# Kernel optimization log

Measured on AMD Instinct MI355X. Metric: run time of the kernel, lower is better.

The kernel has to match this reference:

```python
import jax, jax.numpy as jnp
import numpy as np

NUM_HEADS = 8
WIN = 7  # local_window_size
HALF = WIN // 2


def setup_inputs() -> dict:
    key = jax.random.key(0)
    k1, k2, k3 = jax.random.split(key, 3)
    B, N, C = 1, 4096, 384  # N = T*H*W with T=4, H=W=32
    x = jax.random.normal(k1, (B, N, C), dtype=jnp.float32)
    w_qkv = jax.random.normal(k2, (C, 3 * C), dtype=jnp.float32) * 0.02
    w_proj = jax.random.normal(k3, (C, C), dtype=jnp.float32) * 0.02
    b_proj = jnp.zeros((C,), dtype=jnp.float32)
    return {"x": x, "w_qkv": w_qkv, "w_proj": w_proj, "b_proj": b_proj, "H": 32, "W": 32}


def _gather_windows(t):
    H, W = t.shape[3], t.shape[4]
    tp = jnp.pad(t, ((0, 0), (0, 0), (0, 0), (HALF, HALF), (HALF, HALF), (0, 0)))
    wins = [tp[:, :, :, dy:dy + H, dx:dx + W, :] for dy in range(WIN) for dx in range(WIN)]
    return jnp.stack(wins, axis=5)


def reference(x, w_qkv, w_proj, b_proj, H, W):
    B, N, C = x.shape
    nh, hd = NUM_HEADS, C // NUM_HEADS
    T = N // (H * W)
    scale = hd ** (-0.5)

    qkv = (x @ w_qkv).reshape(B, N, 3, nh, hd)
    # (B, nh, T, H, W, hd)
    q = qkv[:, :, 0].transpose(0, 2, 1, 3).reshape(B, nh, T, H, W, hd)
    k = qkv[:, :, 1].transpose(0, 2, 1, 3).reshape(B, nh, T, H, W, hd)
    v = qkv[:, :, 2].transpose(0, 2, 1, 3).reshape(B, nh, T, H, W, hd)

    kwin = _gather_windows(k)  # (B, nh, T, H, W, 49, hd); zeros at borders (NOT masked)
    vwin = _gather_windows(v)

    scores = jnp.einsum('bnthwd,bnthwkd->bnthwk', q, kwin) * scale
    attn = jax.nn.softmax(scores, axis=-1)  # zero-padded keys give score 0 -> weight exp(0)
    out = jnp.einsum('bnthwk,bnthwkd->bnthwd', attn, vwin)

    out = out.transpose(0, 2, 3, 4, 1, 5).reshape(B, N, C)
    return out @ w_proj + b_proj
```

## Files before the change

kernel.cpp:

```cpp
#include <hip/hip_runtime.h>
#include <hip/hip_bf16.h>
#include <math.h>

#define NH 8
#define HD 48
#define C_DIM 384
#define C3 1152
#define SCALE_F 0.14433756729740643f

typedef unsigned short ushort_t;
typedef __attribute__((ext_vector_type(8))) short short8;
typedef __attribute__((ext_vector_type(4))) float f32x4;

static __device__ __forceinline__ ushort_t bf16u(float f) {
    __hip_bfloat16 b = __float2bfloat16(f);
    return *(ushort_t*)&b;
}

__global__ __launch_bounds__(256) void split_bf16_kernel(const float* __restrict__ in,
                                                         ushort_t* __restrict__ hi,
                                                         ushort_t* __restrict__ lo,
                                                         int n4)
{
    const int i = blockIdx.x * 256 + threadIdx.x;
    if (i >= n4) return;
    const float4 v = ((const float4*)in)[i];
    const float f[4] = {v.x, v.y, v.z, v.w};
    ushort_t hb[4], lb[4];
    #pragma unroll
    for (int j = 0; j < 4; ++j) {
        __hip_bfloat16 h = __float2bfloat16(f[j]);
        __hip_bfloat16 l = __float2bfloat16(f[j] - __bfloat162float(h));
        hb[j] = *(ushort_t*)&h;
        lb[j] = *(ushort_t*)&l;
    }
    *(ushort4*)(hi + i * 4) = make_ushort4(hb[0], hb[1], hb[2], hb[3]);
    *(ushort4*)(lo + i * 4) = make_ushort4(lb[0], lb[1], lb[2], lb[3]);
}

__global__ __launch_bounds__(256) void split_wT_kernel(const float* __restrict__ w,
                                                       ushort_t* __restrict__ hiT,
                                                       ushort_t* __restrict__ loT,
                                                       int K, int N)
{
    const int idx = blockIdx.x * 256 + threadIdx.x;
    if (idx >= K * N) return;
    const int k = idx / N;
    const int n = idx - k * N;
    const float v = w[idx];
    __hip_bfloat16 h = __float2bfloat16(v);
    __hip_bfloat16 l = __float2bfloat16(v - __bfloat162float(h));
    hiT[n * K + k] = *(ushort_t*)&h;
    loT[n * K + k] = *(ushort_t*)&l;
}

__global__ __launch_bounds__(256) void gemm_mfma3(const ushort_t* __restrict__ Ah,
                                                  const ushort_t* __restrict__ Al,
                                                  const ushort_t* __restrict__ BhT,
                                                  const ushort_t* __restrict__ BlT,
                                                  const float* __restrict__ bias,
                                                  float* __restrict__ C,
                                                  int N, int K)
{
    __shared__ ushort_t sAh[128 * 40];
    __shared__ ushort_t sAl[128 * 40];
    __shared__ ushort_t sBh[64 * 40];
    __shared__ ushort_t sBl[64 * 40];

    const int tid = threadIdx.x;
    const int bm = blockIdx.x * 128;
    const int bn = blockIdx.y * 64;

    const int rowA = tid >> 2;
    const int slotA = (tid & 3) * 8;
    const int rowB = tid >> 2;
    const int slotB = (tid & 3) * 8;

    const ushort_t* gAh0 = Ah + (size_t)(bm + rowA) * K + slotA;
    const ushort_t* gAh1 = Ah + (size_t)(bm + rowA + 64) * K + slotA;
    const ushort_t* gAl0 = Al + (size_t)(bm + rowA) * K + slotA;
    const ushort_t* gAl1 = Al + (size_t)(bm + rowA + 64) * K + slotA;
    const ushort_t* gBh  = BhT + (size_t)(bn + rowB) * K + slotB;
    const ushort_t* gBl  = BlT + (size_t)(bn + rowB) * K + slotB;

    const int lane = tid & 63;
    const int wid = tid >> 6;
    const int wm = wid >> 1;
    const int wn = wid & 1;
    const int fr = lane & 15;
    const int kb = lane >> 4;
    const int aoff = (wm * 64 + fr) * 40 + kb * 8;
    const int boff = (wn * 32 + fr) * 40 + kb * 8;

    f32x4 acc[4][2] = {};

    for (int k0 = 0; k0 < K; k0 += 32) {
        const short8 va0 = *(const short8*)(gAh0 + k0);
        const short8 va1 = *(const short8*)(gAh1 + k0);
        const short8 vl0 = *(const short8*)(gAl0 + k0);
        const short8 vl1 = *(const short8*)(gAl1 + k0);
        const short8 vb0 = *(const short8*)(gBh + k0);
        const short8 vb1 = *(const short8*)(gBl + k0);
        *(short8*)&sAh[rowA * 40 + slotA]        = va0;
        *(short8*)&sAh[(rowA + 64) * 40 + slotA] = va1;
        *(short8*)&sAl[rowA * 40 + slotA]        = vl0;
        *(short8*)&sAl[(rowA + 64) * 40 + slotA] = vl1;
        *(short8*)&sBh[rowB * 40 + slotB]        = vb0;
        *(short8*)&sBl[rowB * 40 + slotB]        = vb1;
        __syncthreads();

        short8 ah[4], al[4], bh[2], bl[2];
        #pragma unroll
        for (int m = 0; m < 4; ++m) {
            ah[m] = *(const short8*)&sAh[aoff + m * 16 * 40];
            al[m] = *(const short8*)&sAl[aoff + m * 16 * 40];
        }
        #pragma unroll
        for (int n = 0; n < 2; ++n) {
            bh[n] = *(const short8*)&sBh[boff + n * 16 * 40];
            bl[n] = *(const short8*)&sBl[boff + n * 16 * 40];
        }
        #pragma unroll
        for (int m = 0; m < 4; ++m) {
            #pragma unroll
            for (int n = 0; n < 2; ++n) {
                acc[m][n] = __builtin_amdgcn_mfma_f32_16x16x32_bf16(ah[m], bh[n], acc[m][n], 0, 0, 0);
                acc[m][n] = __builtin_amdgcn_mfma_f32_16x16x32_bf16(ah[m], bl[n], acc[m][n], 0, 0, 0);
                acc[m][n] = __builtin_amdgcn_mfma_f32_16x16x32_bf16(al[m], bh[n], acc[m][n], 0, 0, 0);
            }
        }
        __syncthreads();
    }

    #pragma unroll
    for (int n = 0; n < 2; ++n) {
        const int col = bn + wn * 32 + n * 16 + fr;
        const float bv = bias ? bias[col] : 0.f;
        #pragma unroll
        for (int m = 0; m < 4; ++m) {
            const int r0 = bm + wm * 64 + m * 16 + kb * 4;
            #pragma unroll
            for (int r = 0; r < 4; ++r) {
                C[(size_t)(r0 + r) * N + col] = acc[m][n][r] + bv;
            }
        }
    }
}

__global__ __launch_bounds__(256) void gemm64(const float* __restrict__ A,
                                              const float* __restrict__ B,
                                              const float* __restrict__ bias,
                                              float* __restrict__ C,
                                              int M, int N, int K)
{
    __shared__ float As[64][17];
    __shared__ float Bs[16][64];

    const int tid = threadIdx.x;
    const int tx = tid & 15;
    const int ty = tid >> 4;
    const int bm = blockIdx.x * 64;
    const int bn = blockIdx.y * 64;
    const int arow = tid >> 2;
    const int acol = (tid & 3) << 2;
    const int brow = tid >> 4;
    const int bcol = (tid & 15) << 2;

    float acc[4][4] = {};

    for (int k0 = 0; k0 < K; k0 += 16) {
        const float4 a4 = *(const float4*)(A + (size_t)(bm + arow) * K + k0 + acol);
        const float4 b4 = *(const float4*)(B + (size_t)(k0 + brow) * N + bn + bcol);
        As[arow][acol + 0] = a4.x; As[arow][acol + 1] = a4.y;
        As[arow][acol + 2] = a4.z; As[arow][acol + 3] = a4.w;
        *(float4*)&Bs[brow][bcol] = b4;
        __syncthreads();
        #pragma unroll
        for (int kk = 0; kk < 16; ++kk) {
            const float a0 = As[ty * 4 + 0][kk];
            const float a1 = As[ty * 4 + 1][kk];
            const float a2 = As[ty * 4 + 2][kk];
            const float a3 = As[ty * 4 + 3][kk];
            const float4 b = *(const float4*)&Bs[kk][tx * 4];
            acc[0][0] = fmaf(a0, b.x, acc[0][0]); acc[0][1] = fmaf(a0, b.y, acc[0][1]);
            acc[0][2] = fmaf(a0, b.z, acc[0][2]); acc[0][3] = fmaf(a0, b.w, acc[0][3]);
            acc[1][0] = fmaf(a1, b.x, acc[1][0]); acc[1][1] = fmaf(a1, b.y, acc[1][1]);
            acc[1][2] = fmaf(a1, b.z, acc[1][2]); acc[1][3] = fmaf(a1, b.w, acc[1][3]);
            acc[2][0] = fmaf(a2, b.x, acc[2][0]); acc[2][1] = fmaf(a2, b.y, acc[2][1]);
            acc[2][2] = fmaf(a2, b.z, acc[2][2]); acc[2][3] = fmaf(a2, b.w, acc[2][3]);
            acc[3][0] = fmaf(a3, b.x, acc[3][0]); acc[3][1] = fmaf(a3, b.y, acc[3][1]);
            acc[3][2] = fmaf(a3, b.z, acc[3][2]); acc[3][3] = fmaf(a3, b.w, acc[3][3]);
        }
        __syncthreads();
    }

    float4 bb = {0.f, 0.f, 0.f, 0.f};
    if (bias) bb = *(const float4*)(bias + bn + tx * 4);
    #pragma unroll
    for (int i = 0; i < 4; ++i) {
        float4 o;
        o.x = acc[i][0] + bb.x; o.y = acc[i][1] + bb.y;
        o.z = acc[i][2] + bb.z; o.w = acc[i][3] + bb.w;
        *(float4*)(C + (size_t)(bm + ty * 4 + i) * N + bn + tx * 4) = o;
    }
}

#define KP_SHORTS 18432
#define PROW 72
__global__ __launch_bounds__(512) void local_attn_mfma4(const float* __restrict__ qkv,
                                                        ushort_t* __restrict__ outHi,
                                                        ushort_t* __restrict__ outLo)
{
    __shared__ ushort_t sKP[KP_SHORTS];
    __shared__ ushort_t sV[13504];
    __shared__ ushort_t sQ[2048];
    __shared__ float    sS[32 * 57];

    const int tid = threadIdx.x;
    const int b = blockIdx.x;
    const int t = b >> 8, h = (b >> 3) & 31, head = b & 7;

    if (tid < 288) {
        if (tid < 256) ((unsigned int*)(sKP + 17920))[tid] = 0u;
        else           ((unsigned int*)(sV + 13440))[tid - 256] = 0u;
    }

    #pragma unroll
    for (int it = 0; it < 2; ++it) {
        const int i = tid + it * 512;
        const int q = i >> 5, d = (i & 31) * 2;
        float2 v = make_float2(0.f, 0.f);
        if (d < 48)
            v = *(const float2*)(qkv + (size_t)((t << 10) + (h << 5) + q) * C3 + head * HD + d);
        const unsigned int pk = (unsigned int)bf16u(v.x * SCALE_F) | ((unsigned int)bf16u(v.y * SCALE_F) << 16);
        *(unsigned int*)&sQ[q * 64 + (d ^ ((q & 7) << 3))] = pk;
    }
    #pragma unroll
    for (int r = 0; r < 7; ++r) {
        const int hk = h + r - 3;
        const bool rowok = (unsigned)hk < 32u;
        const size_t rk = (size_t)((t << 10) + (hk << 5)) * C3 + C_DIM + head * HD;
        for (int i = tid; i < 1280; i += 512) {
            const int slot = i >> 5, d = (i & 31) * 2;
            const int c = slot - 3;
            float2 v = make_float2(0.f, 0.f);
            if (rowok && (unsigned)c < 32u && d < 48)
                v = *(const float2*)(qkv + rk + (size_t)c * C3 + d);
            const unsigned int pk = (unsigned int)bf16u(v.x) | ((unsigned int)bf16u(v.y) << 16);
            *(unsigned int*)&sKP[(r * 40 + slot) * 64 + (d ^ ((slot & 7) << 3))] = pk;
        }
    }
    #pragma unroll
    for (int r = 0; r < 7; ++r) {
        const int hk = h + r - 3;
        const bool rowok = (unsigned)hk < 32u;
        const size_t rv = (size_t)((t << 10) + (hk << 5)) * C3 + 2 * C_DIM + head * HD;
        for (int i = tid; i < 960; i += 512) {
            const int slot = i / 24;
            const int d = (i - slot * 24) * 2;
            const int c = slot - 3;
            float2 v = make_float2(0.f, 0.f);
            if (rowok && (unsigned)c < 32u)
                v = *(const float2*)(qkv + rv + (size_t)c * C3 + d);
            sV[(r * 48 + d) * 40 + slot]     = bf16u(v.x);
            sV[(r * 48 + d + 1) * 40 + slot] = bf16u(v.y);
        }
    }
    __syncthreads();

    const int wv = tid >> 6, l = tid & 63, lr = l & 15, lc = l >> 4;

    {
        short8 aq[2][2];
        #pragma unroll
        for (int fm = 0; fm < 2; ++fm) {
            const int q = fm * 16 + lr;
            aq[fm][0] = *(const short8*)&sQ[q * 64 + ((lc * 8) ^ ((q & 7) << 3))];
            aq[fm][1] = *(const short8*)&sQ[q * 64 + ((lc * 8 + 32) ^ ((q & 7) << 3))];
        }
        for (int u = wv; u < 21; u += 8) {
            const int r = u / 3, fn = u - r * 3;
            const int slot = fn * 16 + lr;
            const short8 b0 = *(const short8*)&sKP[(r * 40 + slot) * 64 + ((lc * 8) ^ ((slot & 7) << 3))];
            const short8 b1 = *(const short8*)&sKP[(r * 40 + slot) * 64 + ((lc * 8 + 32) ^ ((slot & 7) << 3))];
            f32x4 acc0 = {}, acc1 = {};
            acc0 = __builtin_amdgcn_mfma_f32_16x16x32_bf16(aq[0][0], b0, acc0, 0, 0, 0);
            acc0 = __builtin_amdgcn_mfma_f32_16x16x32_bf16(aq[0][1], b1, acc0, 0, 0, 0);
            acc1 = __builtin_amdgcn_mfma_f32_16x16x32_bf16(aq[1][0], b0, acc1, 0, 0, 0);
            acc1 = __builtin_amdgcn_mfma_f32_16x16x32_bf16(aq[1][1], b1, acc1, 0, 0, 0);
            #pragma unroll
            for (int reg = 0; reg < 4; ++reg) {
                const int q0 = lc * 4 + reg;
                const int dx0 = slot - q0;
                if (dx0 >= 0 && dx0 < 7) sS[q0 * 57 + r * 7 + dx0] = acc0[reg];
                const int q1 = 16 + lc * 4 + reg;
                const int dx1 = slot - q1;
                if (dx1 >= 0 && dx1 < 7) sS[q1 * 57 + r * 7 + dx1] = acc1[reg];
            }
        }
    }
    __syncthreads();

    if (tid < 32) {
        const int q = tid;
        float sv[49];
        #pragma unroll
        for (int j = 0; j < 49; ++j) sv[j] = sS[q * 57 + j];
        float mx = sv[0];
        #pragma unroll
        for (int j = 1; j < 49; ++j) mx = fmaxf(mx, sv[j]);
        float sum = 0.f;
        #pragma unroll
        for (int j = 0; j < 49; ++j) { sv[j] = __expf(sv[j] - mx); sum += sv[j]; }
        const float inv = 1.f / sum;
        #pragma unroll
        for (int j = 0; j < 49; ++j) {
            const int r = j / 7, dx = j - (j / 7) * 7;
            sKP[(r * 32 + q) * PROW + q + dx] = bf16u(sv[j] * inv);
        }
    } else {
        for (int i = tid - 32; i < 7 * 32 * PROW; i += 480) {
            const int row = i / PROW;
            const int col = i - row * PROW;
            const int q = row & 31;
            if ((unsigned)(col - q) >= 7u)
                sKP[i] = 0;
        }
    }
    __syncthreads();

    if (wv < 6) {
        const int fm = (wv >= 3) ? 1 : 0;
        const int fn = wv - fm * 3;
        const int q = fm * 16 + lr;
        const int dim = fn * 16 + lr;
        f32x4 acc = {};
        #pragma unroll
        for (int r = 0; r < 7; ++r) {
            const short8 a0 = *(const short8*)&sKP[(r * 32 + q) * PROW + lc * 8];
            const short8 a1 = *(const short8*)&sKP[(r * 32 + q) * PROW + lc * 8 + 32];
            const short8 b0 = *(const short8*)&sV[(r * 48 + dim) * 40 + lc * 8];
            const short8 b1 = *(const short8*)&sV[(r * 48 + dim) * 40 + lc * 8 + 32];
            acc = __builtin_amdgcn_mfma_f32_16x16x32_bf16(a0, b0, acc, 0, 0, 0);
            acc = __builtin_amdgcn_mfma_f32_16x16x32_bf16(a1, b1, acc, 0, 0, 0);
        }
        #pragma unroll
        for (int reg = 0; reg < 4; ++reg) {
            const int qq = fm * 16 + lc * 4 + reg;
            const int n = (t << 10) | (h << 5) | qq;
            const float o = acc[reg];
            __hip_bfloat16 hb = __float2bfloat16(o);
            __hip_bfloat16 lb = __float2bfloat16(o - __bfloat162float(hb));
            const size_t ob = (size_t)n * C_DIM + head * HD + dim;
            outHi[ob] = *(ushort_t*)&hb;
            outLo[ob] = *(ushort_t*)&lb;
        }
    }
}

__global__ __launch_bounds__(256) void local_attn16(const float* __restrict__ qkv,
                                                    float* __restrict__ out)
{
    const int tid = threadIdx.x;
    const int dlane = tid & 15;
    const int gid = blockIdx.x * 16 + (tid >> 4);
    const int head = gid & 7;
    const int n = gid >> 3;
    const int t = n >> 10;
    const int h = (n >> 5) & 31;
    const int w = n & 31;
    const float scale = SCALE_F;

    const float* qp = qkv + (size_t)n * C3 + head * HD;
    const float q0 = qp[dlane];
    const float q1 = qp[dlane + 16];
    const float q2 = qp[dlane + 32];

    const size_t base_k = (size_t)(C_DIM + head * HD);
    const size_t base_v = (size_t)(2 * C_DIM + head * HD);

    float s[49];
    #pragma unroll
    for (int p = 0; p < 49; ++p) {
        const int dy = p / 7, dx = p % 7;
        const int hk = h + dy - 3;
        const int wk = w + dx - 3;
        float sc = 0.f;
        if ((unsigned)hk < 32u && (unsigned)wk < 32u) {
            const int nk = (t << 10) | (hk << 5) | wk;
            const float* kp = qkv + (size_t)nk * C3 + base_k;
            float acc = q0 * kp[dlane];
            acc = fmaf(q1, kp[dlane + 16], acc);
            acc = fmaf(q2, kp[dlane + 32], acc);
            acc += __shfl_xor(acc, 1, 16);
            acc += __shfl_xor(acc, 2, 16);
            acc += __shfl_xor(acc, 4, 16);
            acc += __shfl_xor(acc, 8, 16);
            sc = acc * scale;
        }
        s[p] = sc;
    }

    float m = s[0];
    #pragma unroll
    for (int p = 1; p < 49; ++p) m = fmaxf(m, s[p]);
    float sum = 0.f;
    #pragma unroll
    for (int p = 0; p < 49; ++p) { s[p] = __expf(s[p] - m); sum += s[p]; }
    const float inv = 1.f / sum;

    float o0 = 0.f, o1 = 0.f, o2 = 0.f;
    #pragma unroll
    for (int p = 0; p < 49; ++p) {
        const int dy = p / 7, dx = p % 7;
        const int hk = h + dy - 3;
        const int wk = w + dx - 3;
        if ((unsigned)hk < 32u && (unsigned)wk < 32u) {
            const float wgt = s[p] * inv;
            const int nk = (t << 10) | (hk << 5) | wk;
            const float* vp = qkv + (size_t)nk * C3 + base_v;
            o0 = fmaf(wgt, vp[dlane],      o0);
            o1 = fmaf(wgt, vp[dlane + 16], o1);
            o2 = fmaf(wgt, vp[dlane + 32], o2);
        }
    }

    float* op = out + (size_t)n * C_DIM + head * HD;
    op[dlane]      = o0;
    op[dlane + 16] = o1;
    op[dlane + 32] = o2;
}

extern "C" void kernel_launch(void* const* d_in, const int* in_sizes, int n_in,
                              void* d_out, int out_size, void* d_ws, size_t ws_size,
                              hipStream_t stream)
{
    const float* x      = (const float*)d_in[0];
    const float* w_qkv  = (const float*)d_in[1];
    const float* w_proj = (const float*)d_in[2];
    const float* b_proj = (const float*)d_in[3];

    const int M = 4096;
    dim3 blk(256);

    const size_t NEED = 33226752;

    unsigned char* ws = (unsigned char*)d_ws;
    float* qkv = (float*)ws;
    float* att = (float*)(ws + 18874368);

    if (ws_size >= NEED) {
        ushort_t* Ah  = (ushort_t*)(ws + 25165824);
        ushort_t* Al  = (ushort_t*)(ws + 28311552);
        ushort_t* BhT = (ushort_t*)(ws + 31457280);
        ushort_t* BlT = (ushort_t*)(ws + 32342016);

        split_bf16_kernel<<<dim3(1536), blk, 0, stream>>>(x, Ah, Al, M * C_DIM / 4);
        split_wT_kernel<<<dim3((C_DIM * C3 + 255) / 256), blk, 0, stream>>>(w_qkv, BhT, BlT, C_DIM, C3);
        gemm_mfma3<<<dim3(M / 128, C3 / 64), blk, 0, stream>>>(Ah, Al, BhT, BlT, nullptr, qkv, C3, C_DIM);

        local_attn_mfma4<<<dim3(1024), dim3(512), 0, stream>>>(qkv, Ah, Al);

        split_wT_kernel<<<dim3((C_DIM * C_DIM + 255) / 256), blk, 0, stream>>>(w_proj, BhT, BlT, C_DIM, C_DIM);
        gemm_mfma3<<<dim3(M / 128, C_DIM / 64), blk, 0, stream>>>(Ah, Al, BhT, BlT, b_proj, (float*)d_out, C_DIM, C_DIM);
    } else {
        gemm64<<<dim3(M / 64, C3 / 64), blk, 0, stream>>>(x, w_qkv, nullptr, qkv, M, C3, C_DIM);
        local_attn16<<<dim3(2048), blk, 0, stream>>>(qkv, att);
        gemm64<<<dim3(M / 64, C_DIM / 64), blk, 0, stream>>>(att, w_proj, b_proj, (float*)d_out, M, C_DIM, C_DIM);
    }
}
```

Baseline: 91.92 us.

## Widen QKV GEMM tile to 128x128 and overlap V loads with QK MFMA

```diff
diff --git a/kernel.cpp b/kernel.cpp
--- a/kernel.cpp
+++ b/kernel.cpp
@@ -147,6 +147,89 @@
     }
 }
 
+__global__ __launch_bounds__(512) void gemm_mfma3w(const ushort_t* __restrict__ Ah,
+                                                   const ushort_t* __restrict__ Al,
+                                                   const ushort_t* __restrict__ BhT,
+                                                   const ushort_t* __restrict__ BlT,
+                                                   float* __restrict__ C,
+                                                   int N, int K)
+{
+    __shared__ ushort_t sAh[128 * 40];
+    __shared__ ushort_t sAl[128 * 40];
+    __shared__ ushort_t sBh[128 * 40];
+    __shared__ ushort_t sBl[128 * 40];
+
+    const int tid = threadIdx.x;
+    const int bm = blockIdx.x * 128;
+    const int bn = blockIdx.y * 128;
+
+    const int rowA = tid >> 2;
+    const int slotA = (tid & 3) * 8;
+
+    const ushort_t* gAh = Ah + (size_t)(bm + rowA) * K + slotA;
+    const ushort_t* gAl = Al + (size_t)(bm + rowA) * K + slotA;
+    const ushort_t* gBh = BhT + (size_t)(bn + rowA) * K + slotA;
+    const ushort_t* gBl = BlT + (size_t)(bn + rowA) * K + slotA;
+
+    const int lane = tid & 63;
+    const int wid = tid >> 6;
+    const int wm = wid >> 2;
+    const int wn = wid & 3;
+    const int fr = lane & 15;
+    const int kb = lane >> 4;
+    const int aoff = (wm * 64 + fr) * 40 + kb * 8;
+    const int boff = (wn * 32 + fr) * 40 + kb * 8;
+
+    f32x4 acc[4][2] = {};
+
+    for (int k0 = 0; k0 < K; k0 += 32) {
+        const short8 va = *(const short8*)(gAh + k0);
+        const short8 vl = *(const short8*)(gAl + k0);
+        const short8 vb = *(const short8*)(gBh + k0);
+        const short8 vc = *(const short8*)(gBl + k0);
+        *(short8*)&sAh[rowA * 40 + slotA] = va;
+        *(short8*)&sAl[rowA * 40 + slotA] = vl;
+        *(short8*)&sBh[rowA * 40 + slotA] = vb;
+        *(short8*)&sBl[rowA * 40 + slotA] = vc;
+        __syncthreads();
+
+        short8 ah[4], al[4], bh[2], bl[2];
+        #pragma unroll
+        for (int m = 0; m < 4; ++m) {
+            ah[m] = *(const short8*)&sAh[aoff + m * 16 * 40];
+            al[m] = *(const short8*)&sAl[aoff + m * 16 * 40];
+        }
+        #pragma unroll
+        for (int n = 0; n < 2; ++n) {
+            bh[n] = *(const short8*)&sBh[boff + n * 16 * 40];
+            bl[n] = *(const short8*)&sBl[boff + n * 16 * 40];
+        }
+        #pragma unroll
+        for (int m = 0; m < 4; ++m) {
+            #pragma unroll
+            for (int n = 0; n < 2; ++n) {
+                acc[m][n] = __builtin_amdgcn_mfma_f32_16x16x32_bf16(ah[m], bh[n], acc[m][n], 0, 0, 0);
+                acc[m][n] = __builtin_amdgcn_mfma_f32_16x16x32_bf16(ah[m], bl[n], acc[m][n], 0, 0, 0);
+                acc[m][n] = __builtin_amdgcn_mfma_f32_16x16x32_bf16(al[m], bh[n], acc[m][n], 0, 0, 0);
+            }
+        }
+        __syncthreads();
+    }
+
+    #pragma unroll
+    for (int n = 0; n < 2; ++n) {
+        const int col = bn + wn * 32 + n * 16 + fr;
+        #pragma unroll
+        for (int m = 0; m < 4; ++m) {
+            const int r0 = bm + wm * 64 + m * 16 + kb * 4;
+            #pragma unroll
+            for (int r = 0; r < 4; ++r) {
+                C[(size_t)(r0 + r) * N + col] = acc[m][n][r];
+            }
+        }
+    }
+}
+
 __global__ __launch_bounds__(256) void gemm64(const float* __restrict__ A,
                                               const float* __restrict__ B,
                                               const float* __restrict__ bias,
@@ -207,7 +290,7 @@
 
 #define KP_SHORTS 18432
 #define PROW 72
-__global__ __launch_bounds__(512) void local_attn_mfma4(const float* __restrict__ qkv,
+__global__ __launch_bounds__(512) void local_attn_mfma5(const float* __restrict__ qkv,
                                                         ushort_t* __restrict__ outHi,
                                                         ushort_t* __restrict__ outLo)
 {
@@ -250,26 +333,30 @@
             *(unsigned int*)&sKP[(r * 40 + slot) * 64 + (d ^ ((slot & 7) << 3))] = pk;
         }
     }
+    __syncthreads();
+
+    const int wv = tid >> 6, l = tid & 63, lr = l & 15, lc = l >> 4;
+
+    float2 vreg[7][2];
     #pragma unroll
     for (int r = 0; r < 7; ++r) {
         const int hk = h + r - 3;
         const bool rowok = (unsigned)hk < 32u;
         const size_t rv = (size_t)((t << 10) + (hk << 5)) * C3 + 2 * C_DIM + head * HD;
-        for (int i = tid; i < 960; i += 512) {
-            const int slot = i / 24;
-            const int d = (i - slot * 24) * 2;
-            const int c = slot - 3;
+        #pragma unroll
+        for (int it = 0; it < 2; ++it) {
+            const int i = tid + it * 512;
             float2 v = make_float2(0.f, 0.f);
-            if (rowok && (unsigned)c < 32u)
-                v = *(const float2*)(qkv + rv + (size_t)c * C3 + d);
-            sV[(r * 48 + d) * 40 + slot]     = bf16u(v.x);
-            sV[(r * 48 + d + 1) * 40 + slot] = bf16u(v.y);
-        }
-    }
-    __syncthreads();
-
-    const int wv = tid >> 6, l = tid & 63, lr = l & 15, lc = l >> 4;
-
+            if (i < 960) {
+                const int slot = i / 24;
+                const int d = (i - slot * 24) * 2;
+                const int c = slot - 3;
+                if (rowok && (unsigned)c < 32u)
+                    v = *(const float2*)(qkv + rv + (size_t)c * C3 + d);
+            }
+            vreg[r][it] = v;
+        }
+    }
     {
         short8 aq[2][2];
         #pragma unroll
@@ -301,6 +388,19 @@
     }
     __syncthreads();
 
+    #pragma unroll
+    for (int r = 0; r < 7; ++r) {
+        #pragma unroll
+        for (int it = 0; it < 2; ++it) {
+            const int i = tid + it * 512;
+            if (i < 960) {
+                const int slot = i / 24;
+                const int d = (i - slot * 24) * 2;
+                sV[(r * 48 + d) * 40 + slot]     = bf16u(vreg[r][it].x);
+                sV[(r * 48 + d + 1) * 40 + slot] = bf16u(vreg[r][it].y);
+            }
+        }
+    }
     if (tid < 32) {
         const int q = tid;
         float sv[49];
@@ -457,9 +557,9 @@
 
         split_bf16_kernel<<<dim3(1536), blk, 0, stream>>>(x, Ah, Al, M * C_DIM / 4);
         split_wT_kernel<<<dim3((C_DIM * C3 + 255) / 256), blk, 0, stream>>>(w_qkv, BhT, BlT, C_DIM, C3);
-        gemm_mfma3<<<dim3(M / 128, C3 / 64), blk, 0, stream>>>(Ah, Al, BhT, BlT, nullptr, qkv, C3, C_DIM);
-
-        local_attn_mfma4<<<dim3(1024), dim3(512), 0, stream>>>(qkv, Ah, Al);
+        gemm_mfma3w<<<dim3(M / 128, C3 / 128), dim3(512), 0, stream>>>(Ah, Al, BhT, BlT, qkv, C3, C_DIM);
+
+        local_attn_mfma5<<<dim3(1024), dim3(512), 0, stream>>>(qkv, Ah, Al);
 
         split_wT_kernel<<<dim3((C_DIM * C_DIM + 255) / 256), blk, 0, stream>>>(w_proj, BhT, BlT, C_DIM, C_DIM);
         gemm_mfma3<<<dim3(M / 128, C_DIM / 64), blk, 0, stream>>>(Ah, Al, BhT, BlT, b_proj, (float*)d_out, C_DIM, C_DIM);
```

Result: slower. 95.00 us (+3.4%).
